# Performance work log

Measured on AMD Instinct MI355X. Metric: run time of the kernel, lower is better.

## Reference

```python
import jax, jax.numpy as jnp
import numpy as np

K, D, B = 8192, 512, 8192

def setup_inputs() -> dict:
    key = jax.random.key(0)
    k1, k2, k3 = jax.random.split(key, 3)
    z_e_x = jax.random.normal(k1, (B, 2 * D), dtype=jnp.float32)
    # torch init: uniform_(-1/K, 1/K)
    W_a = jax.random.uniform(k2, (K, D), minval=-1.0 / K, maxval=1.0 / K, dtype=jnp.float32)
    W_v = jax.random.uniform(k3, (K, D), minval=-1.0 / K, maxval=1.0 / K, dtype=jnp.float32)
    return {"z_e_x": z_e_x, "W_a": W_a, "W_v": W_v}

def _straight_through(z, W):
    # z: [B, D], W: [K, D]
    Wd = jax.lax.stop_gradient(W)        # weight.detach()
    scores = jnp.einsum('bd,kd->bk', z, Wd)  # [B, K] (returned as 'indices' in the original)
    idx = jnp.argmax(scores, axis=-1)    # [B]
    z_q_st = Wd[idx]                     # gather from detached weight
    z_q = W[idx]                         # gather from live weight
    return z_q_st, z_q, scores

def reference(z_e_x, W_a, W_v):
    d = W_a.shape[1]
    st_a, q_a, s_a = _straight_through(z_e_x[:, :d], W_a)
    st_v, q_v, s_v = _straight_through(z_e_x[:, d:], W_v)
    z_q_x_st = jnp.concatenate([st_a, st_v], axis=-1)  # [B, 2D]
    z_q_x = jnp.concatenate([q_a, q_v], axis=-1)       # [B, 2D]
    indices = jnp.concatenate([s_a, s_v], axis=-1)     # [B, 2K] raw scores, per original
    return (z_q_x_st, z_q_x, indices)
```

## Files before the change

### kernel.cpp

```cpp
#include <hip/hip_runtime.h>
#include <stdint.h>


namespace {
constexpr int D     = 512;
constexpr int TWO_D = 1024;
constexpr int K     = 8192;
constexpr int B     = 8192;
constexpr int BM = 128, BN = 128, BK = 32;
constexpr int NCHUNK = D / BK;
}

typedef __attribute__((ext_vector_type(8))) short short8;
typedef __attribute__((ext_vector_type(4))) float f32x4;

__device__ __forceinline__ unsigned int score_key(float s) {
    unsigned int u = __float_as_uint(s);
    return (u & 0x80000000u) ? ~u : (u | 0x80000000u);
}

__device__ __forceinline__ unsigned long long shfl_xor_u64(unsigned long long v, int m) {
    unsigned int hi = (unsigned int)(v >> 32), lo = (unsigned int)v;
    hi = __shfl_xor(hi, m, 64);
    lo = __shfl_xor(lo, m, 64);
    return ((unsigned long long)hi << 32) | lo;
}

__device__ __forceinline__ void cvt_pair(float x0, float x1, unsigned &hiw, unsigned &low) {
    unsigned u0 = __float_as_uint(x0), u1 = __float_as_uint(x1);
    hiw = (u0 >> 16) | (u1 & 0xFFFF0000u);
    float l0 = x0 - __uint_as_float(u0 & 0xFFFF0000u);
    float l1 = x1 - __uint_as_float(u1 & 0xFFFF0000u);
    asm("v_cvt_pk_bf16_f32 %0, %1, %2" : "=v"(low) : "v"(l0), "v"(l1));
}

__device__ __forceinline__ void cvt8(float4 a, float4 b, uint4 &h, uint4 &l) {
    cvt_pair(a.x, a.y, h.x, l.x);
    cvt_pair(a.z, a.w, h.y, l.y);
    cvt_pair(b.x, b.y, h.z, l.z);
    cvt_pair(b.z, b.w, h.w, l.w);
}

__global__ void init_ws_kernel(unsigned long long* __restrict__ ws) {
    int i = blockIdx.x * blockDim.x + threadIdx.x;
    if (i < 4 * B) ws[i] = 0ull;
}

__global__ __launch_bounds__(256, 2) void gemm_argmax_kernel(
    const float* __restrict__ z,
    const float* __restrict__ Wa,
    const float* __restrict__ Wv,
    float* __restrict__ scores,
    unsigned long long* __restrict__ slot1,
    unsigned long long* __restrict__ slot2)
{
    __shared__ uint4 smem4[2048];
    char* smem = (char*)smem4;
    constexpr int AHI = 0, ALO = 8192, BHI = 16384, BLO = 24576;

    const int h = blockIdx.z;
    const float* __restrict__ W = h ? Wv : Wa;

    int id = blockIdx.y * 64 + blockIdx.x;
    id = (id & 7) * 512 + (id >> 3);
    const int rowBase = (id >> 6) * BM;
    const int colBase = (id & 63) * BN;

    const int tid  = threadIdx.x;
    const int lane = tid & 63;
    const int wv   = tid >> 6;
    const int wr   = wv >> 1, wc = wv & 1;
    const int fr   = lane & 15, fq = lane >> 4;

    const int sr = tid >> 1;
    const int sk = (tid & 1) << 4;
    const int c0 = (tid & 1) << 1;
    const int swzr = sr & 3;
    const int wb0 = sr * 64 + (((c0 + 0) ^ swzr) << 4);
    const int wb1 = sr * 64 + (((c0 + 1) ^ swzr) << 4);

    const float* zp = z + (size_t)(rowBase + sr) * TWO_D + h * D + sk;
    const float* wp = W + (size_t)(colBase + sr) * D + sk;

    const int swzc = (fq ^ (fr & 3)) << 4;
    const int aOff = (wr * 64 + fr) * 64 + swzc;
    const int bOff = (wc * 64 + fr) * 64 + swzc;

    f32x4 acc[4][4];
#pragma unroll
    for (int m = 0; m < 4; ++m)
#pragma unroll
        for (int n = 0; n < 4; ++n) acc[m][n] = (f32x4){0.f, 0.f, 0.f, 0.f};

    float4 a0, a1, a2, a3, b0, b1, b2, b3;
    a0 = *(const float4*)(zp + 0);  a1 = *(const float4*)(zp + 4);
    a2 = *(const float4*)(zp + 8);  a3 = *(const float4*)(zp + 12);
    b0 = *(const float4*)(wp + 0);  b1 = *(const float4*)(wp + 4);
    b2 = *(const float4*)(wp + 8);  b3 = *(const float4*)(wp + 12);

    for (int kc = 0; kc < NCHUNK; ++kc) {
        uint4 ah0, ah1, al0, al1, bh0, bh1, bl0, bl1;
        cvt8(a0, a1, ah0, al0);
        cvt8(a2, a3, ah1, al1);
        cvt8(b0, b1, bh0, bl0);
        cvt8(b2, b3, bh1, bl1);

        __syncthreads();
        *(uint4*)(smem + AHI + wb0) = ah0;
        *(uint4*)(smem + AHI + wb1) = ah1;
        *(uint4*)(smem + ALO + wb0) = al0;
        *(uint4*)(smem + ALO + wb1) = al1;
        *(uint4*)(smem + BHI + wb0) = bh0;
        *(uint4*)(smem + BHI + wb1) = bh1;
        *(uint4*)(smem + BLO + wb0) = bl0;
        *(uint4*)(smem + BLO + wb1) = bl1;
        __syncthreads();

        if (kc + 1 < NCHUNK) {
            const float* zn = zp + (kc + 1) * BK;
            const float* wn = wp + (kc + 1) * BK;
            a0 = *(const float4*)(zn + 0);  a1 = *(const float4*)(zn + 4);
            a2 = *(const float4*)(zn + 8);  a3 = *(const float4*)(zn + 12);
            b0 = *(const float4*)(wn + 0);  b1 = *(const float4*)(wn + 4);
            b2 = *(const float4*)(wn + 8);  b3 = *(const float4*)(wn + 12);
        }

        short8 ah[4], al[4], bh[4], bl[4];
#pragma unroll
        for (int m = 0; m < 4; ++m) {
            ah[m] = *(const short8*)(smem + AHI + aOff + m * 1024);
            al[m] = *(const short8*)(smem + ALO + aOff + m * 1024);
        }
#pragma unroll
        for (int n = 0; n < 4; ++n) {
            bh[n] = *(const short8*)(smem + BHI + bOff + n * 1024);
            bl[n] = *(const short8*)(smem + BLO + bOff + n * 1024);
        }
#pragma unroll
        for (int m = 0; m < 4; ++m)
#pragma unroll
            for (int n = 0; n < 4; ++n) {
                acc[m][n] = __builtin_amdgcn_mfma_f32_16x16x32_bf16(ah[m], bh[n], acc[m][n], 0, 0, 0);
                acc[m][n] = __builtin_amdgcn_mfma_f32_16x16x32_bf16(al[m], bh[n], acc[m][n], 0, 0, 0);
                acc[m][n] = __builtin_amdgcn_mfma_f32_16x16x32_bf16(ah[m], bl[n], acc[m][n], 0, 0, 0);
            }
    }

#pragma unroll
    for (int m = 0; m < 4; ++m) {
#pragma unroll
        for (int jj = 0; jj < 4; ++jj) {
            const int R = rowBase + wr * 64 + m * 16 + fq * 4 + jj;
            float* sp = scores + (size_t)R * (2 * K) + (size_t)h * K + colBase + wc * 64 + fr;
            unsigned long long best = 0ull, second = 0ull;
#pragma unroll
            for (int n = 0; n < 4; ++n) {
                const float v = acc[m][n][jj];
                sp[n * 16] = v;
                const int col = colBase + wc * 64 + n * 16 + fr;
                unsigned long long p =
                    ((unsigned long long)score_key(v) << 32) |
                    (unsigned long long)(0xFFFFFFFFu - (unsigned)col);
                if (p > best) { second = best; best = p; }
                else if (p > second) { second = p; }
            }
#pragma unroll
            for (int w = 1; w < 16; w <<= 1) {
                unsigned long long ob = shfl_xor_u64(best, w);
                unsigned long long os = shfl_xor_u64(second, w);
                unsigned long long nb = best > ob ? best : ob;
                unsigned long long lose = best > ob ? ob : best;
                unsigned long long s2 = second > os ? second : os;
                best = nb;
                second = lose > s2 ? lose : s2;
            }
            if (fr == 0) {
                unsigned long long* s1p = slot1 + (size_t)h * B + R;
                unsigned long long old = atomicMax(s1p, best);
                unsigned long long cand = old < best ? old : best;
                if (second > cand) cand = second;
                atomicMax(slot2 + (size_t)h * B + R, cand);
            }
        }
    }
}

__global__ __launch_bounds__(256) void fixup_kernel(
    const float* __restrict__ z, const float* __restrict__ Wa,
    const float* __restrict__ Wv, unsigned long long* __restrict__ ws)
{
    const int gid  = blockIdx.x * 4 + (threadIdx.x >> 6);
    const int lane = threadIdx.x & 63;
    const int h    = gid >> 13;
    const int row  = gid & (B - 1);
    const unsigned long long* slot1 = ws;
    const unsigned long long* slot2 = ws + 2 * B;
    unsigned int* idxArr = (unsigned int*)(ws + 4 * B);

    const size_t sb = (size_t)h * B + row;
    const unsigned c1 = 0xFFFFFFFFu - (unsigned)(slot1[sb] & 0xFFFFFFFFull);
    const unsigned c2 = 0xFFFFFFFFu - (unsigned)(slot2[sb] & 0xFFFFFFFFull);
    const float* Wm = h ? Wv : Wa;
    const float* zr = z + (size_t)row * TWO_D + h * D;
    const float* w1 = Wm + (size_t)c1 * D;
    const float* w2 = Wm + (size_t)c2 * D;

    const int k0 = lane * 8;
    float4 za = *(const float4*)(zr + k0);
    float4 zb = *(const float4*)(zr + k0 + 4);
    float4 p  = *(const float4*)(w1 + k0);
    float4 q  = *(const float4*)(w1 + k0 + 4);
    float4 r  = *(const float4*)(w2 + k0);
    float4 s  = *(const float4*)(w2 + k0 + 4);

    float d1 = 0.f, d2 = 0.f;
    d1 = fmaf(za.x, p.x, d1); d1 = fmaf(za.y, p.y, d1);
    d1 = fmaf(za.z, p.z, d1); d1 = fmaf(za.w, p.w, d1);
    d1 = fmaf(zb.x, q.x, d1); d1 = fmaf(zb.y, q.y, d1);
    d1 = fmaf(zb.z, q.z, d1); d1 = fmaf(zb.w, q.w, d1);
    d2 = fmaf(za.x, r.x, d2); d2 = fmaf(za.y, r.y, d2);
    d2 = fmaf(za.z, r.z, d2); d2 = fmaf(za.w, r.w, d2);
    d2 = fmaf(zb.x, s.x, d2); d2 = fmaf(zb.y, s.y, d2);
    d2 = fmaf(zb.z, s.z, d2); d2 = fmaf(zb.w, s.w, d2);

#pragma unroll
    for (int m = 1; m < 64; m <<= 1) {
        d1 += __shfl_xor(d1, m, 64);
        d2 += __shfl_xor(d2, m, 64);
    }
    if (lane == 0)
        idxArr[sb] = (d2 > d1 || (d2 == d1 && c2 < c1)) ? c2 : c1;
}

__global__ __launch_bounds__(256) void gather_kernel(
    const float* __restrict__ Wa, const float* __restrict__ Wv,
    const unsigned long long* __restrict__ ws,
    float* __restrict__ out0, float* __restrict__ out1)
{
    const unsigned int* idxArr = (const unsigned int*)(ws + 4 * B);
    const int b = blockIdx.x;
    const int t = threadIdx.x;
    const unsigned ia = idxArr[b];
    const unsigned iv = idxArr[B + b];

    const float* src;
    size_t dst;
    if (t < 128) {
        src = Wa + (size_t)ia * D + t * 4;
        dst = (size_t)b * TWO_D + t * 4;
    } else {
        src = Wv + (size_t)iv * D + (t - 128) * 4;
        dst = (size_t)b * TWO_D + D + (t - 128) * 4;
    }
    float4 v = *(const float4*)src;
    *(float4*)(out0 + dst) = v;
    *(float4*)(out1 + dst) = v;
}

extern "C" void kernel_launch(void* const* d_in, const int* in_sizes, int n_in,
                              void* d_out, int out_size, void* d_ws, size_t ws_size,
                              hipStream_t stream) {
    const float* z  = (const float*)d_in[0];
    const float* Wa = (const float*)d_in[1];
    const float* Wv = (const float*)d_in[2];

    float* out0   = (float*)d_out;
    float* out1   = out0 + (size_t)B * TWO_D;
    float* scores = out1 + (size_t)B * TWO_D;

    unsigned long long* ws = (unsigned long long*)d_ws;

    hipLaunchKernelGGL(init_ws_kernel, dim3((4 * B + 255) / 256), dim3(256), 0, stream, ws);
    hipLaunchKernelGGL(gemm_argmax_kernel, dim3(K / BN, B / BM, 2), dim3(256), 0, stream,
                       z, Wa, Wv, scores, ws, ws + 2 * (size_t)B);
    hipLaunchKernelGGL(fixup_kernel, dim3(2 * B / 4), dim3(256), 0, stream, z, Wa, Wv, ws);
    hipLaunchKernelGGL(gather_kernel, dim3(B), dim3(256), 0, stream, Wa, Wv, ws, out0, out1);
}
```

Baseline: 1.342 ms.

## Pre-split operands to bf16 hi/lo tiles and stream via global_load_lds

Adds a pre-pass kernel that converts z and both codebooks into swizzled bf16 hi/lo tiles, staged in the output buffers as scratch. The GEMM then loads these tiles straight into LDS with global_load_lds, with no per-block fp32 conversion and no register round trip. This removes the conversion work that was repeated across the 64 column/row blocks that reuse each tile, and lets the next chunk load overlap the MFMAs. The costs are an extra pass over the inputs, a higher occupancy target, and nontemporal stores for the scores.

```diff
diff --git a/kernel.cpp b/kernel.cpp
--- a/kernel.cpp
+++ b/kernel.cpp
@@ -9,10 +9,17 @@
 constexpr int B     = 8192;
 constexpr int BM = 128, BN = 128, BK = 32;
 constexpr int NCHUNK = D / BK;
+constexpr size_t LO_OFF = 8388608;
 }
 
 typedef __attribute__((ext_vector_type(8))) short short8;
 typedef __attribute__((ext_vector_type(4))) float f32x4;
+typedef __attribute__((address_space(1))) const unsigned int GU32;
+typedef __attribute__((address_space(3))) unsigned int LU32;
+
+__device__ __forceinline__ void gload_lds16(const void* g, void* l) {
+    __builtin_amdgcn_global_load_lds((GU32*)g, (LU32*)l, 16, 0, 0);
+}
 
 __device__ __forceinline__ unsigned int score_key(float s) {
     unsigned int u = __float_as_uint(s);
@@ -46,25 +53,68 @@
     if (i < 4 * B) ws[i] = 0ull;
 }
 
-__global__ __launch_bounds__(256, 2) void gemm_argmax_kernel(
-    const float* __restrict__ z,
-    const float* __restrict__ Wa,
+__global__ __launch_bounds__(256) void split_kernel(
+    const float* __restrict__ z, const float* __restrict__ Wa,
     const float* __restrict__ Wv,
+    uint16_t* __restrict__ zs,
+    uint16_t* __restrict__ wsp)
+{
+    const int bid = blockIdx.x;
+    const bool isW = bid >= 2048;
+    const int t  = bid & 2047;
+    const int h  = t >> 10;
+    const int rb = (t >> 4) & 63;
+    const int kc = t & 15;
+    const int t2 = threadIdx.x;
+    const int r  = t2 >> 1;
+    const int kh = (t2 & 1) << 4;
+
+    const float* src;
+    uint16_t* base;
+    if (!isW) {
+        src  = z + (size_t)(rb * 128 + r) * TWO_D + h * D + kc * 32 + kh;
+        base = zs;
+    } else {
+        const float* W = h ? Wv : Wa;
+        src  = W + (size_t)(rb * 128 + r) * D + kc * 32 + kh;
+        base = wsp;
+    }
+    const size_t tbase = ((size_t)(h * 64 + rb) * 16 + kc) * 4096;
+
+    float4 f0 = ((const float4*)src)[0], f1 = ((const float4*)src)[1];
+    float4 f2 = ((const float4*)src)[2], f3 = ((const float4*)src)[3];
+    uint4 hch[2], lch[2];
+    cvt8(f0, f1, hch[0], lch[0]);
+    cvt8(f2, f3, hch[1], lch[1]);
+
+    const int swzr = r & 3;
+    const int c0 = (t2 & 1) * 2;
+#pragma unroll
+    for (int j = 0; j < 2; ++j) {
+        const int cpos = (c0 + j) ^ swzr;
+        const size_t off = tbase + (size_t)r * 32 + cpos * 8;
+        *(uint4*)(base + off)          = hch[j];
+        *(uint4*)(base + LO_OFF + off) = lch[j];
+    }
+}
+
+__global__ __launch_bounds__(256, 3) void gemm_argmax_kernel(
+    const uint16_t* __restrict__ zs,
+    const uint16_t* __restrict__ wsp,
     float* __restrict__ scores,
     unsigned long long* __restrict__ slot1,
     unsigned long long* __restrict__ slot2)
 {
-    __shared__ uint4 smem4[2048];
-    char* smem = (char*)smem4;
-    constexpr int AHI = 0, ALO = 8192, BHI = 16384, BLO = 24576;
+    __shared__ __align__(16) uint16_t smem[16384];
+    char* sm = (char*)smem;
 
     const int h = blockIdx.z;
-    const float* __restrict__ W = h ? Wv : Wa;
-
     int id = blockIdx.y * 64 + blockIdx.x;
     id = (id & 7) * 512 + (id >> 3);
-    const int rowBase = (id >> 6) * BM;
-    const int colBase = (id & 63) * BN;
+    const int rb = id >> 6;
+    const int cb = id & 63;
+    const int rowBase = rb * BM;
+    const int colBase = cb * BN;
 
     const int tid  = threadIdx.x;
     const int lane = tid & 63;
@@ -72,19 +122,12 @@
     const int wr   = wv >> 1, wc = wv & 1;
     const int fr   = lane & 15, fq = lane >> 4;
 
-    const int sr = tid >> 1;
-    const int sk = (tid & 1) << 4;
-    const int c0 = (tid & 1) << 1;
-    const int swzr = sr & 3;
-    const int wb0 = sr * 64 + (((c0 + 0) ^ swzr) << 4);
-    const int wb1 = sr * 64 + (((c0 + 1) ^ swzr) << 4);
-
-    const float* zp = z + (size_t)(rowBase + sr) * TWO_D + h * D + sk;
-    const float* wp = W + (size_t)(colBase + sr) * D + sk;
-
-    const int swzc = (fq ^ (fr & 3)) << 4;
-    const int aOff = (wr * 64 + fr) * 64 + swzc;
-    const int bOff = (wc * 64 + fr) * 64 + swzc;
+    const size_t zhib = (size_t)(h * 64 + rb) * 16 * 4096;
+    const size_t whib = (size_t)(h * 64 + cb) * 16 * 4096;
+
+    const int swzc  = (fq ^ (fr & 3)) << 4;
+    const int aByte = (wr * 64 + fr) * 64 + swzc;
+    const int bByte = (wc * 64 + fr) * 64 + swzc;
 
     f32x4 acc[4][4];
 #pragma unroll
@@ -92,50 +135,38 @@
 #pragma unroll
         for (int n = 0; n < 4; ++n) acc[m][n] = (f32x4){0.f, 0.f, 0.f, 0.f};
 
-    float4 a0, a1, a2, a3, b0, b1, b2, b3;
-    a0 = *(const float4*)(zp + 0);  a1 = *(const float4*)(zp + 4);
-    a2 = *(const float4*)(zp + 8);  a3 = *(const float4*)(zp + 12);
-    b0 = *(const float4*)(wp + 0);  b1 = *(const float4*)(wp + 4);
-    b2 = *(const float4*)(wp + 8);  b3 = *(const float4*)(wp + 12);
+    auto STAGE = [&](int kc) {
+        const uint16_t* za = zs  + zhib + (size_t)kc * 4096 + wv * 1024 + lane * 8;
+        const uint16_t* wa = wsp + whib + (size_t)kc * 4096 + wv * 1024 + lane * 8;
+        char* lb = sm + wv * 2048;
+        gload_lds16(za,                lb);
+        gload_lds16(za + 512,          lb + 1024);
+        gload_lds16(za + LO_OFF,       lb + 8192);
+        gload_lds16(za + LO_OFF + 512, lb + 8192 + 1024);
+        gload_lds16(wa,                lb + 16384);
+        gload_lds16(wa + 512,          lb + 16384 + 1024);
+        gload_lds16(wa + LO_OFF,       lb + 24576);
+        gload_lds16(wa + LO_OFF + 512, lb + 24576 + 1024);
+    };
+
+    STAGE(0);
+    __syncthreads();
 
     for (int kc = 0; kc < NCHUNK; ++kc) {
-        uint4 ah0, ah1, al0, al1, bh0, bh1, bl0, bl1;
-        cvt8(a0, a1, ah0, al0);
-        cvt8(a2, a3, ah1, al1);
-        cvt8(b0, b1, bh0, bl0);
-        cvt8(b2, b3, bh1, bl1);
-
+        short8 ah[4], al[4], bh[4], bl[4];
+#pragma unroll
+        for (int m = 0; m < 4; ++m) {
+            ah[m] = *(const short8*)(sm +         aByte + m * 1024);
+            al[m] = *(const short8*)(sm + 8192  + aByte + m * 1024);
+        }
+#pragma unroll
+        for (int n = 0; n < 4; ++n) {
+            bh[n] = *(const short8*)(sm + 16384 + bByte + n * 1024);
+            bl[n] = *(const short8*)(sm + 24576 + bByte + n * 1024);
+        }
         __syncthreads();
-        *(uint4*)(smem + AHI + wb0) = ah0;
-        *(uint4*)(smem + AHI + wb1) = ah1;
-        *(uint4*)(smem + ALO + wb0) = al0;
-        *(uint4*)(smem + ALO + wb1) = al1;
-        *(uint4*)(smem + BHI + wb0) = bh0;
-        *(uint4*)(smem + BHI + wb1) = bh1;
-        *(uint4*)(smem + BLO + wb0) = bl0;
-        *(uint4*)(smem + BLO + wb1) = bl1;
-        __syncthreads();
-
-        if (kc + 1 < NCHUNK) {
-            const float* zn = zp + (kc + 1) * BK;
-            const float* wn = wp + (kc + 1) * BK;
-            a0 = *(const float4*)(zn + 0);  a1 = *(const float4*)(zn + 4);
-            a2 = *(const float4*)(zn + 8);  a3 = *(const float4*)(zn + 12);
-            b0 = *(const float4*)(wn + 0);  b1 = *(const float4*)(wn + 4);
-            b2 = *(const float4*)(wn + 8);  b3 = *(const float4*)(wn + 12);
-        }
-
-        short8 ah[4], al[4], bh[4], bl[4];
-#pragma unroll
-        for (int m = 0; m < 4; ++m) {
-            ah[m] = *(const short8*)(smem + AHI + aOff + m * 1024);
-            al[m] = *(const short8*)(smem + ALO + aOff + m * 1024);
-        }
-#pragma unroll
-        for (int n = 0; n < 4; ++n) {
-            bh[n] = *(const short8*)(smem + BHI + bOff + n * 1024);
-            bl[n] = *(const short8*)(smem + BLO + bOff + n * 1024);
-        }
+        if (kc + 1 < NCHUNK) STAGE(kc + 1);
+
 #pragma unroll
         for (int m = 0; m < 4; ++m)
 #pragma unroll
@@ -144,6 +175,7 @@
                 acc[m][n] = __builtin_amdgcn_mfma_f32_16x16x32_bf16(al[m], bh[n], acc[m][n], 0, 0, 0);
                 acc[m][n] = __builtin_amdgcn_mfma_f32_16x16x32_bf16(ah[m], bl[n], acc[m][n], 0, 0, 0);
             }
+        __syncthreads();
     }
 
 #pragma unroll
@@ -156,7 +188,7 @@
 #pragma unroll
             for (int n = 0; n < 4; ++n) {
                 const float v = acc[m][n][jj];
-                sp[n * 16] = v;
+                __builtin_nontemporal_store(v, sp + n * 16);
                 const int col = colBase + wc * 64 + n * 16 + fr;
                 unsigned long long p =
                     ((unsigned long long)score_key(v) << 32) |
@@ -268,11 +300,16 @@
     float* out1   = out0 + (size_t)B * TWO_D;
     float* scores = out1 + (size_t)B * TWO_D;
 
+    uint16_t* zsplit = (uint16_t*)out0;
+    uint16_t* wsplit = (uint16_t*)out1;
+
     unsigned long long* ws = (unsigned long long*)d_ws;
 
     hipLaunchKernelGGL(init_ws_kernel, dim3((4 * B + 255) / 256), dim3(256), 0, stream, ws);
+    hipLaunchKernelGGL(split_kernel, dim3(4096), dim3(256), 0, stream,
+                       z, Wa, Wv, zsplit, wsplit);
     hipLaunchKernelGGL(gemm_argmax_kernel, dim3(K / BN, B / BM, 2), dim3(256), 0, stream,
-                       z, Wa, Wv, scores, ws, ws + 2 * (size_t)B);
+                       zsplit, wsplit, scores, ws, ws + 2 * (size_t)B);
     hipLaunchKernelGGL(fixup_kernel, dim3(2 * B / 4), dim3(256), 0, stream, z, Wa, Wv, ws);
     hipLaunchKernelGGL(gather_kernel, dim3(B), dim3(256), 0, stream, Wa, Wv, ws, out0, out1);
 }
```

New measurement: 1.229 ms. -8.5%, faster.
